# Performance work log

Hardware: AMD Instinct MI355X
Metric: run time of the kernel (lower is better)

## Reference

```python
import jax, jax.numpy as jnp
import numpy as np

B, S, D = 2, 2048, 1024
H = 16
HD = D // H  # 64
FORESIGHT = -1e9  # masked_fill value for non-causal positions


def setup_inputs() -> dict:
    key = jax.random.key(0)
    ks = jax.random.split(key, 8)
    s = 0.02
    return {
        "x": jax.random.normal(ks[0], (B, S, D), dtype=jnp.float32),
        "Wq": jax.random.normal(ks[1], (D, H * HD), dtype=jnp.float32) * s,
        "bq": jax.random.normal(ks[2], (H * HD,), dtype=jnp.float32) * s,
        "Wk": jax.random.normal(ks[3], (D, H * HD), dtype=jnp.float32) * s,
        "Wv": jax.random.normal(ks[4], (D, H * HD), dtype=jnp.float32) * s,
        "Wo": jax.random.normal(ks[5], (H * HD, D), dtype=jnp.float32) * s,
        "bo": jax.random.normal(ks[6], (D,), dtype=jnp.float32) * s,
    }


def reference(x, Wq, bq, Wk, Wv, Wo, bo):
    b, s, _ = x.shape
    # projections -> [B, H, S, HD]
    q = (x @ Wq + bq).reshape(b, s, H, HD).transpose(0, 2, 1, 3)
    k = (x @ Wk).reshape(b, s, H, HD).transpose(0, 2, 1, 3)
    v = (x @ Wv).reshape(b, s, H, HD).transpose(0, 2, 1, 3)
    # scores [B, H, S, S]
    scores = jnp.einsum("bhqd,bhkd->bhqk", q, k) / jnp.sqrt(jnp.float32(HD))
    # ALiBi bias: slope_h * j (key position), broadcast over queries
    slopes = 2.0 ** (-8.0 * jnp.arange(1, H + 1, dtype=jnp.float32) / H)
    positions = jnp.arange(s, dtype=jnp.float32)
    scores = scores - slopes[None, :, None, None] * positions[None, None, None, :]
    # causal mask: fill strictly-upper triangle with foresight
    causal = jnp.tril(jnp.ones((s, s), dtype=bool))
    scores = jnp.where(causal[None, None, :, :], scores, FORESIGHT)
    attn = jax.nn.softmax(scores, axis=-1)
    out = jnp.einsum("bhqk,bhkd->bhqd", attn, v)
    out = out.transpose(0, 2, 1, 3).reshape(b, s, H * HD)
    return out @ Wo + bo
```

## Files before the change

kernel.cpp:

```cpp
#include <hip/hip_runtime.h>
#include <stdint.h>

#define DDIM 1024
#define HH 16
#define HDIM 64
#define SS 2048
#define BB 2
#define MTOT 4096

typedef short bf16x8 __attribute__((ext_vector_type(8)));
typedef float f32x4 __attribute__((ext_vector_type(4)));
typedef unsigned short u16;

__device__ __forceinline__ u16 f2bf(float f) {
  unsigned u = __builtin_bit_cast(unsigned, f);
  u = u + 0x7FFFu + ((u >> 16) & 1u);
  return (u16)(u >> 16);
}

__device__ __forceinline__ void gload16(const void* g, void* l) {
  __builtin_amdgcn_global_load_lds(
      (const __attribute__((address_space(1))) unsigned int*)g,
      (__attribute__((address_space(3))) unsigned int*)l, 16, 0, 0);
}

__global__ void k_convert_x(const float* __restrict__ x, u16* __restrict__ xb) {
  int i = (blockIdx.x * 256 + threadIdx.x) * 4;
  float4 v = *(const float4*)(x + i);
  ushort4 o;
  o.x = f2bf(v.x); o.y = f2bf(v.y); o.z = f2bf(v.z); o.w = f2bf(v.w);
  *(ushort4*)(xb + i) = o;
}

__global__ void k_transpose_w(const float* __restrict__ w0, const float* __restrict__ w1,
                              const float* __restrict__ w2, const float* __restrict__ w3,
                              u16* __restrict__ wt) {
  __shared__ float t[64][65];
  int z = blockIdx.z;
  const float* src = (z == 0) ? w0 : (z == 1) ? w1 : (z == 2) ? w2 : w3;
  u16* dst = wt + (size_t)z * DDIM * DDIM;
  int k0 = blockIdx.x * 64, n0 = blockIdx.y * 64;
  int tid = threadIdx.x;
  int c4 = tid & 15, rr = tid >> 4;
  for (int rep = 0; rep < 4; rep++) {
    int r = rr + rep * 16;
    float4 v = *(const float4*)(src + (size_t)(k0 + r) * DDIM + n0 + c4 * 4);
    t[r][c4 * 4 + 0] = v.x; t[r][c4 * 4 + 1] = v.y;
    t[r][c4 * 4 + 2] = v.z; t[r][c4 * 4 + 3] = v.w;
  }
  __syncthreads();
  for (int rep = 0; rep < 4; rep++) {
    int n = rr + rep * 16;
    ushort4 o;
    o.x = f2bf(t[c4 * 4 + 0][n]); o.y = f2bf(t[c4 * 4 + 1][n]);
    o.z = f2bf(t[c4 * 4 + 2][n]); o.w = f2bf(t[c4 * 4 + 3][n]);
    *(ushort4*)(dst + (size_t)(n0 + n) * DDIM + k0 + c4 * 4) = o;
  }
}

template <int MODE>
__global__ __launch_bounds__(256, 2) void k_gemm(const u16* __restrict__ A,
                                                 const u16* __restrict__ BT,
                                                 const float* __restrict__ bias,
                                                 void* __restrict__ Cout) {
  __shared__ __align__(16) u16 lA[128 * 64];
  __shared__ __align__(16) u16 lB[128 * 64];
  const int tid = threadIdx.x;
  const int l = tid & 63, w = tid >> 6;
  const int wm = w >> 1, wn = w & 1;
  const int m0 = blockIdx.x * 128, n0 = blockIdx.y * 128;
  const int lr = l >> 4, lc = l & 15;

  const int srow = l >> 3;
  const int scol = ((l & 7) ^ srow) * 8;

  f32x4 acc[4][4];
  for (int mi = 0; mi < 4; mi++)
    for (int ni = 0; ni < 4; ni++)
      acc[mi][ni] = f32x4{0.f, 0.f, 0.f, 0.f};

  for (int kk = 0; kk < 16; kk++) {
    const int k0 = kk * 64;
    for (int i = 0; i < 4; i++) {
      int c = w * 4 + i;
      gload16(A + (size_t)(m0 + c * 8 + srow) * DDIM + k0 + scol, (char*)lA + c * 1024);
      gload16(BT + (size_t)(n0 + c * 8 + srow) * DDIM + k0 + scol, (char*)lB + c * 1024);
    }
    __syncthreads();
    for (int ks = 0; ks < 2; ks++) {
      bf16x8 af[4], bfr[4];
      for (int mi = 0; mi < 4; mi++) {
        int row = wm * 64 + mi * 16 + lc;
        int slot = (ks * 4 + lr) ^ (row & 7);
        af[mi] = *(const bf16x8*)((const char*)lA + row * 128 + slot * 16);
      }
      for (int ni = 0; ni < 4; ni++) {
        int row = wn * 64 + ni * 16 + lc;
        int slot = (ks * 4 + lr) ^ (row & 7);
        bfr[ni] = *(const bf16x8*)((const char*)lB + row * 128 + slot * 16);
      }
      for (int mi = 0; mi < 4; mi++)
        for (int ni = 0; ni < 4; ni++)
          acc[mi][ni] = __builtin_amdgcn_mfma_f32_16x16x32_bf16(af[mi], bfr[ni], acc[mi][ni], 0, 0, 0);
    }
    __syncthreads();
  }

  if (MODE == 0) {
    u16* C = (u16*)Cout;
    for (int mi = 0; mi < 4; mi++)
      for (int ni = 0; ni < 4; ni++) {
        int n = n0 + wn * 64 + ni * 16 + lc;
        float badd = bias ? bias[n] : 0.f;
        for (int r = 0; r < 4; r++) {
          int m = m0 + wm * 64 + mi * 16 + lr * 4 + r;
          C[(size_t)m * DDIM + n] = f2bf(acc[mi][ni][r] + badd);
        }
      }
  } else if (MODE == 1) {
    u16* C = (u16*)Cout;
    for (int mi = 0; mi < 4; mi++)
      for (int ni = 0; ni < 4; ni++) {
        int n = n0 + wn * 64 + ni * 16 + lc;
        int h = n >> 6, hd = n & 63;
        for (int r = 0; r < 4; r++) {
          int m = m0 + wm * 64 + mi * 16 + lr * 4 + r;
          int b = m >> 11, s = m & 2047;
          C[((size_t)((b * HH + h) * HDIM + hd)) * SS + s] = f2bf(acc[mi][ni][r]);
        }
      }
  } else {
    float* C = (float*)Cout;
    for (int mi = 0; mi < 4; mi++)
      for (int ni = 0; ni < 4; ni++) {
        int n = n0 + wn * 64 + ni * 16 + lc;
        float badd = bias[n];
        for (int r = 0; r < 4; r++) {
          int m = m0 + wm * 64 + mi * 16 + lr * 4 + r;
          C[(size_t)m * DDIM + n] = acc[mi][ni][r] + badd;
        }
      }
  }
}

__global__ __launch_bounds__(256, 3) void k_attn(const u16* __restrict__ Q,
                                                 const u16* __restrict__ Kg,
                                                 const u16* __restrict__ Vt,
                                                 u16* __restrict__ AO) {
  __shared__ __align__(16) u16 lK[128 * 64];
  __shared__ __align__(16) u16 lV[64 * 128];
  __shared__ __align__(16) u16 lP[4][16 * 128];

  const int tid = threadIdx.x;
  const int l = tid & 63, w = tid >> 6;
  const int lr = l >> 4, lc = l & 15;
  const int bh = blockIdx.x;
  const int b = bh >> 4, h = bh & 15;
  const int yq = blockIdx.y;
  const int fk = yq & 7, fj = yq >> 3;
  const int qt = (fj == 0) ? fk : (fj == 1) ? (15 - fk) : (fj == 2) ? (16 + fk) : (31 - fk);

  const float slope = exp2f(-0.5f * (float)(h + 1));
  const int q_glob = qt * 64 + w * 16 + lc;

  bf16x8 qf[2];
  for (int ks = 0; ks < 2; ks++)
    qf[ks] = *(const bf16x8*)(Q + (size_t)(b * SS + q_glob) * DDIM + h * HDIM + ks * 32 + lr * 8);

  f32x4 of[4];
  for (int mf = 0; mf < 4; mf++) of[mf] = f32x4{0.f, 0.f, 0.f, 0.f};
  float mrun = -INFINITY, lrun = 0.f;

  const int srowK = l >> 3;
  const int scolK = ((l & 7) ^ srowK) * 8;
  const int nkt = qt / 2 + 1;

  for (int kt = 0; kt < nkt; kt++) {
    for (int i = 0; i < 4; i++) {
      int c = w * 4 + i;
      int key = kt * 128 + c * 8 + srowK;
      gload16(Kg + (size_t)(b * SS + key) * DDIM + h * HDIM + scolK, (char*)lK + c * 1024);
      int hd = c * 4 + lr;
      int slot = (l & 15) ^ (hd & 7);
      gload16(Vt + ((size_t)bh * HDIM + hd) * SS + kt * 128 + slot * 8, (char*)lV + c * 1024);
    }
    __syncthreads();

    f32x4 sf[8];
    for (int kf = 0; kf < 8; kf++) sf[kf] = f32x4{0.f, 0.f, 0.f, 0.f};
    for (int ks = 0; ks < 2; ks++)
      for (int kf = 0; kf < 8; kf++) {
        int key = kf * 16 + lc;
        int slot = (ks * 4 + lr) ^ (key & 7);
        bf16x8 a = *(const bf16x8*)((const char*)lK + key * 128 + slot * 16);
        sf[kf] = __builtin_amdgcn_mfma_f32_16x16x32_bf16(a, qf[ks], sf[kf], 0, 0, 0);
      }

    float tmax = -INFINITY;
    for (int kf = 0; kf < 8; kf++)
      for (int r = 0; r < 4; r++) {
        int key = kt * 128 + kf * 16 + lr * 4 + r;
        float sv = sf[kf][r] * 0.125f - slope * (float)key;
        sv = (key > q_glob) ? -1e9f : sv;
        sf[kf][r] = sv;
        tmax = fmaxf(tmax, sv);
      }
    tmax = fmaxf(tmax, __shfl_xor(tmax, 16));
    tmax = fmaxf(tmax, __shfl_xor(tmax, 32));
    float mnew = fmaxf(mrun, tmax);
    float scale = __expf(mrun - mnew);
    lrun *= scale;
    for (int mf = 0; mf < 4; mf++)
      for (int r = 0; r < 4; r++) of[mf][r] *= scale;

    float psum = 0.f;
    for (int kf = 0; kf < 8; kf++)
      for (int r = 0; r < 4; r++) {
        float p = __expf(sf[kf][r] - mnew);
        psum += p;
        int key = kf * 16 + lr * 4 + r;
        int slot = (key >> 3) ^ (lc & 7);
        *(u16*)((char*)lP[w] + lc * 256 + slot * 16 + (key & 7) * 2) = f2bf(p);
      }
    psum += __shfl_xor(psum, 16);
    psum += __shfl_xor(psum, 32);
    lrun += psum;
    mrun = mnew;

    for (int ks = 0; ks < 4; ks++) {
      int slotp = (ks * 4 + lr) ^ (lc & 7);
      bf16x8 pb = *(const bf16x8*)((const char*)lP[w] + lc * 256 + slotp * 16);
      for (int mf = 0; mf < 4; mf++) {
        int hd = mf * 16 + lc;
        int slotv = (ks * 4 + lr) ^ (hd & 7);
        bf16x8 va = *(const bf16x8*)((const char*)lV + hd * 256 + slotv * 16);
        of[mf] = __builtin_amdgcn_mfma_f32_16x16x32_bf16(va, pb, of[mf], 0, 0, 0);
      }
    }
    __syncthreads();
  }

  float inv = 1.f / lrun;
  for (int mf = 0; mf < 4; mf++)
    for (int r = 0; r < 4; r++) {
      int hd = mf * 16 + lr * 4 + r;
      AO[(size_t)(b * SS + q_glob) * DDIM + h * HDIM + hd] = f2bf(of[mf][r] * inv);
    }
}

extern "C" void kernel_launch(void* const* d_in, const int* in_sizes, int n_in,
                              void* d_out, int out_size, void* d_ws, size_t ws_size,
                              hipStream_t stream) {
  const float* x  = (const float*)d_in[0];
  const float* Wq = (const float*)d_in[1];
  const float* bq = (const float*)d_in[2];
  const float* Wk = (const float*)d_in[3];
  const float* Wv = (const float*)d_in[4];
  const float* Wo = (const float*)d_in[5];
  const float* bo = (const float*)d_in[6];
  float* out = (float*)d_out;

  u16* ws = (u16*)d_ws;
  const size_t MEG = 1024 * 1024;
  u16* xb = ws;
  u16* WT = ws + 4 * MEG;
  u16* Qb = ws + 8 * MEG;
  u16* Kb = ws + 12 * MEG;
  u16* Vt = ws + 16 * MEG;
  u16* AO = ws + 20 * MEG;

  k_convert_x<<<dim3(4096), dim3(256), 0, stream>>>(x, xb);
  k_transpose_w<<<dim3(16, 16, 4), dim3(256), 0, stream>>>(Wq, Wk, Wv, Wo, WT);
  k_gemm<0><<<dim3(32, 8), dim3(256), 0, stream>>>(xb, WT + 0 * MEG, bq, (void*)Qb);
  k_gemm<0><<<dim3(32, 8), dim3(256), 0, stream>>>(xb, WT + 1 * MEG, (const float*)nullptr, (void*)Kb);
  k_gemm<1><<<dim3(32, 8), dim3(256), 0, stream>>>(xb, WT + 2 * MEG, (const float*)nullptr, (void*)Vt);
  k_attn<<<dim3(32, 32), dim3(256), 0, stream>>>(Qb, Kb, Vt, AO);
  k_gemm<2><<<dim3(32, 8), dim3(256), 0, stream>>>(AO, WT + 3 * MEG, bo, (void*)out);
}
```

Measured before the change: 151.2 us.

## Fuse QKV GEMMs, keep P in registers, skip masked tiles in attention

Merges the three QKV projection launches into one grid of 24 column tiles that writes Q, K and transposed V, with V stored as packed 32-bit pairs. The attention kernel no longer routes P through LDS: it packs the probabilities into bf16x4 registers and feeds them to 16x16x16 MFMAs. Only the last key tile is masked, and for even query tiles half of its key fragments are skipped. The rescale runs only when the running max grows, the output is written with vector stores, and the occupancy hint rises to 4. This cuts kernel launches, LDS traffic and wasted masked work, at the cost of more inline asm and register pressure.

Result: faster. 123.7 us (-18.2%).

```diff
diff --git a/kernel.cpp b/kernel.cpp
--- a/kernel.cpp
+++ b/kernel.cpp
@@ -5,17 +5,20 @@
 #define HH 16
 #define HDIM 64
 #define SS 2048
-#define BB 2
-#define MTOT 4096
 
 typedef short bf16x8 __attribute__((ext_vector_type(8)));
+typedef short bf16x4 __attribute__((ext_vector_type(4)));
 typedef float f32x4 __attribute__((ext_vector_type(4)));
 typedef unsigned short u16;
 
-__device__ __forceinline__ u16 f2bf(float f) {
+__device__ __forceinline__ unsigned f2bf(float f) {
   unsigned u = __builtin_bit_cast(unsigned, f);
   u = u + 0x7FFFu + ((u >> 16) & 1u);
-  return (u16)(u >> 16);
+  return u >> 16;
+}
+
+__device__ __forceinline__ void mfma16(f32x4& c, bf16x4 a, bf16x4 b) {
+  asm("v_mfma_f32_16x16x16_bf16 %0, %1, %2, %0" : "+v"(c) : "v"(a), "v"(b));
 }
 
 __device__ __forceinline__ void gload16(const void* g, void* l) {
@@ -28,7 +31,7 @@
   int i = (blockIdx.x * 256 + threadIdx.x) * 4;
   float4 v = *(const float4*)(x + i);
   ushort4 o;
-  o.x = f2bf(v.x); o.y = f2bf(v.y); o.z = f2bf(v.z); o.w = f2bf(v.w);
+  o.x = (u16)f2bf(v.x); o.y = (u16)f2bf(v.y); o.z = (u16)f2bf(v.z); o.w = (u16)f2bf(v.w);
   *(ushort4*)(xb + i) = o;
 }
 
@@ -52,8 +55,8 @@
   for (int rep = 0; rep < 4; rep++) {
     int n = rr + rep * 16;
     ushort4 o;
-    o.x = f2bf(t[c4 * 4 + 0][n]); o.y = f2bf(t[c4 * 4 + 1][n]);
-    o.z = f2bf(t[c4 * 4 + 2][n]); o.w = f2bf(t[c4 * 4 + 3][n]);
+    o.x = (u16)f2bf(t[c4 * 4 + 0][n]); o.y = (u16)f2bf(t[c4 * 4 + 1][n]);
+    o.z = (u16)f2bf(t[c4 * 4 + 2][n]); o.w = (u16)f2bf(t[c4 * 4 + 3][n]);
     *(ushort4*)(dst + (size_t)(n0 + n) * DDIM + k0 + c4 * 4) = o;
   }
 }
@@ -62,7 +65,9 @@
 __global__ __launch_bounds__(256, 2) void k_gemm(const u16* __restrict__ A,
                                                  const u16* __restrict__ BT,
                                                  const float* __restrict__ bias,
-                                                 void* __restrict__ Cout) {
+                                                 void* __restrict__ O0,
+                                                 void* __restrict__ O1,
+                                                 void* __restrict__ O2) {
   __shared__ __align__(16) u16 lA[128 * 64];
   __shared__ __align__(16) u16 lB[128 * 64];
   const int tid = threadIdx.x;
@@ -107,30 +112,45 @@
   }
 
   if (MODE == 0) {
-    u16* C = (u16*)Cout;
-    for (int mi = 0; mi < 4; mi++)
-      for (int ni = 0; ni < 4; ni++) {
-        int n = n0 + wn * 64 + ni * 16 + lc;
-        float badd = bias ? bias[n] : 0.f;
-        for (int r = 0; r < 4; r++) {
-          int m = m0 + wm * 64 + mi * 16 + lr * 4 + r;
-          C[(size_t)m * DDIM + n] = f2bf(acc[mi][ni][r] + badd);
+    const int which = blockIdx.y >> 3;
+    if (which == 0) {
+      u16* C = (u16*)O0;
+      for (int mi = 0; mi < 4; mi++)
+        for (int ni = 0; ni < 4; ni++) {
+          int nl = (n0 + wn * 64 + ni * 16 + lc) & 1023;
+          float badd = bias[nl];
+          for (int r = 0; r < 4; r++) {
+            int m = m0 + wm * 64 + mi * 16 + lr * 4 + r;
+            C[(size_t)m * DDIM + nl] = (u16)f2bf(acc[mi][ni][r] + badd);
+          }
         }
-      }
-  } else if (MODE == 1) {
-    u16* C = (u16*)Cout;
-    for (int mi = 0; mi < 4; mi++)
-      for (int ni = 0; ni < 4; ni++) {
-        int n = n0 + wn * 64 + ni * 16 + lc;
-        int h = n >> 6, hd = n & 63;
-        for (int r = 0; r < 4; r++) {
-          int m = m0 + wm * 64 + mi * 16 + lr * 4 + r;
+    } else if (which == 1) {
+      u16* C = (u16*)O1;
+      for (int mi = 0; mi < 4; mi++)
+        for (int ni = 0; ni < 4; ni++) {
+          int nl = (n0 + wn * 64 + ni * 16 + lc) & 1023;
+          for (int r = 0; r < 4; r++) {
+            int m = m0 + wm * 64 + mi * 16 + lr * 4 + r;
+            C[(size_t)m * DDIM + nl] = (u16)f2bf(acc[mi][ni][r]);
+          }
+        }
+    } else {
+      u16* C = (u16*)O2;
+      for (int mi = 0; mi < 4; mi++)
+        for (int ni = 0; ni < 4; ni++) {
+          int nl = (n0 + wn * 64 + ni * 16 + lc) & 1023;
+          int h = nl >> 6, hd = nl & 63;
+          int m = m0 + wm * 64 + mi * 16 + lr * 4;
           int b = m >> 11, s = m & 2047;
-          C[((size_t)((b * HH + h) * HDIM + hd)) * SS + s] = f2bf(acc[mi][ni][r]);
+          unsigned d0 = f2bf(acc[mi][ni][0]) | (f2bf(acc[mi][ni][1]) << 16);
+          unsigned d1 = f2bf(acc[mi][ni][2]) | (f2bf(acc[mi][ni][3]) << 16);
+          u16* p = C + ((size_t)((b * HH + h) * HDIM + hd)) * SS + s;
+          *(unsigned*)(p) = d0;
+          *(unsigned*)(p + 2) = d1;
         }
-      }
+    }
   } else {
-    float* C = (float*)Cout;
+    float* C = (float*)O0;
     for (int mi = 0; mi < 4; mi++)
       for (int ni = 0; ni < 4; ni++) {
         int n = n0 + wn * 64 + ni * 16 + lc;
@@ -143,13 +163,94 @@
   }
 }
 
-__global__ __launch_bounds__(256, 3) void k_attn(const u16* __restrict__ Q,
+__device__ __forceinline__ void attn_tile(int kt, bool masked, int kfhi,
+                                          const char* lKc, const char* lVc,
+                                          const bf16x8 qf[2], f32x4 of[4],
+                                          float& mrun, float& lrun,
+                                          float slope, int lr, int lc, int q_glob) {
+  f32x4 sf[8];
+#pragma unroll
+  for (int kf = 0; kf < 8; kf++) sf[kf] = f32x4{0.f, 0.f, 0.f, 0.f};
+#pragma unroll
+  for (int ks = 0; ks < 2; ks++)
+#pragma unroll
+    for (int kf = 0; kf < 8; kf++) {
+      if (kf >= kfhi) continue;
+      int key = kf * 16 + lc;
+      int slot = (ks * 4 + lr) ^ (lc & 7);
+      bf16x8 a = *(const bf16x8*)(lKc + key * 128 + slot * 16);
+      sf[kf] = __builtin_amdgcn_mfma_f32_16x16x32_bf16(a, qf[ks], sf[kf], 0, 0, 0);
+    }
+
+  float tmax = -INFINITY;
+#pragma unroll
+  for (int kf = 0; kf < 8; kf++) {
+    if (kf >= kfhi) continue;
+#pragma unroll
+    for (int r = 0; r < 4; r++) {
+      int key = kt * 128 + kf * 16 + lr * 4 + r;
+      float sv = sf[kf][r] * 0.125f - slope * (float)key;
+      if (masked && key > q_glob) sv = -1e9f;
+      sf[kf][r] = sv;
+      tmax = fmaxf(tmax, sv);
+    }
+  }
+  tmax = fmaxf(tmax, __shfl_xor(tmax, 16));
+  tmax = fmaxf(tmax, __shfl_xor(tmax, 32));
+
+  if (tmax > mrun) {
+    float corr = __expf(mrun - tmax);
+    lrun *= corr;
+#pragma unroll
+    for (int mf = 0; mf < 4; mf++) {
+      of[mf][0] *= corr; of[mf][1] *= corr; of[mf][2] *= corr; of[mf][3] *= corr;
+    }
+    mrun = tmax;
+  }
+
+  f32x4 ps = f32x4{0.f, 0.f, 0.f, 0.f};
+  bf16x4 pb[8];
+#pragma unroll
+  for (int kf = 0; kf < 8; kf++) {
+    if (kf >= kfhi) continue;
+    unsigned a0 = f2bf(__expf(sf[kf][0] - mrun));
+    unsigned a1 = f2bf(__expf(sf[kf][1] - mrun));
+    unsigned a2 = f2bf(__expf(sf[kf][2] - mrun));
+    unsigned a3 = f2bf(__expf(sf[kf][3] - mrun));
+    uint2 uu;
+    uu.x = a0 | (a1 << 16);
+    uu.y = a2 | (a3 << 16);
+    pb[kf] = __builtin_bit_cast(bf16x4, uu);
+    ps[0] += __builtin_bit_cast(float, a0 << 16);
+    ps[1] += __builtin_bit_cast(float, a1 << 16);
+    ps[2] += __builtin_bit_cast(float, a2 << 16);
+    ps[3] += __builtin_bit_cast(float, a3 << 16);
+  }
+  float psum = (ps[0] + ps[1]) + (ps[2] + ps[3]);
+  psum += __shfl_xor(psum, 16);
+  psum += __shfl_xor(psum, 32);
+  lrun += psum;
+
+#pragma unroll
+  for (int kf = 0; kf < 8; kf++) {
+    if (kf >= kfhi) continue;
+    int g2 = (kf << 1) + (lr >> 1);
+#pragma unroll
+    for (int mf = 0; mf < 4; mf++) {
+      int hd = mf * 16 + lc;
+      int byte = hd * 256 + ((g2 ^ (hd & 7)) << 4) + ((lr & 1) << 3);
+      bf16x4 va = *(const bf16x4*)(lVc + byte);
+      mfma16(of[mf], va, pb[kf]);
+    }
+  }
+}
+
+__global__ __launch_bounds__(256, 4) void k_attn(const u16* __restrict__ Q,
                                                  const u16* __restrict__ Kg,
                                                  const u16* __restrict__ Vt,
                                                  u16* __restrict__ AO) {
   __shared__ __align__(16) u16 lK[128 * 64];
   __shared__ __align__(16) u16 lV[64 * 128];
-  __shared__ __align__(16) u16 lP[4][16 * 128];
 
   const int tid = threadIdx.x;
   const int l = tid & 63, w = tid >> 6;
@@ -164,10 +265,12 @@
   const int q_glob = qt * 64 + w * 16 + lc;
 
   bf16x8 qf[2];
+#pragma unroll
   for (int ks = 0; ks < 2; ks++)
     qf[ks] = *(const bf16x8*)(Q + (size_t)(b * SS + q_glob) * DDIM + h * HDIM + ks * 32 + lr * 8);
 
   f32x4 of[4];
+#pragma unroll
   for (int mf = 0; mf < 4; mf++) of[mf] = f32x4{0.f, 0.f, 0.f, 0.f};
   float mrun = -INFINITY, lrun = 0.f;
 
@@ -175,77 +278,43 @@
   const int scolK = ((l & 7) ^ srowK) * 8;
   const int nkt = qt / 2 + 1;
 
-  for (int kt = 0; kt < nkt; kt++) {
+  auto stage = [&](int kt) {
+#pragma unroll
     for (int i = 0; i < 4; i++) {
       int c = w * 4 + i;
-      int key = kt * 128 + c * 8 + srowK;
-      gload16(Kg + (size_t)(b * SS + key) * DDIM + h * HDIM + scolK, (char*)lK + c * 1024);
+      gload16(Kg + (size_t)(b * SS + kt * 128 + c * 8 + srowK) * DDIM + h * HDIM + scolK,
+              (char*)lK + c * 1024);
       int hd = c * 4 + lr;
-      int slot = (l & 15) ^ (hd & 7);
-      gload16(Vt + ((size_t)bh * HDIM + hd) * SS + kt * 128 + slot * 8, (char*)lV + c * 1024);
-    }
+      gload16(Vt + ((size_t)bh * HDIM + hd) * SS + kt * 128 + (((l & 15) ^ (hd & 7)) << 3),
+              (char*)lV + c * 1024);
+    }
+  };
+
+  for (int kt = 0; kt < nkt - 1; kt++) {
+    stage(kt);
     __syncthreads();
-
-    f32x4 sf[8];
-    for (int kf = 0; kf < 8; kf++) sf[kf] = f32x4{0.f, 0.f, 0.f, 0.f};
-    for (int ks = 0; ks < 2; ks++)
-      for (int kf = 0; kf < 8; kf++) {
-        int key = kf * 16 + lc;
-        int slot = (ks * 4 + lr) ^ (key & 7);
-        bf16x8 a = *(const bf16x8*)((const char*)lK + key * 128 + slot * 16);
-        sf[kf] = __builtin_amdgcn_mfma_f32_16x16x32_bf16(a, qf[ks], sf[kf], 0, 0, 0);
-      }
-
-    float tmax = -INFINITY;
-    for (int kf = 0; kf < 8; kf++)
-      for (int r = 0; r < 4; r++) {
-        int key = kt * 128 + kf * 16 + lr * 4 + r;
-        float sv = sf[kf][r] * 0.125f - slope * (float)key;
-        sv = (key > q_glob) ? -1e9f : sv;
-        sf[kf][r] = sv;
-        tmax = fmaxf(tmax, sv);
-      }
-    tmax = fmaxf(tmax, __shfl_xor(tmax, 16));
-    tmax = fmaxf(tmax, __shfl_xor(tmax, 32));
-    float mnew = fmaxf(mrun, tmax);
-    float scale = __expf(mrun - mnew);
-    lrun *= scale;
-    for (int mf = 0; mf < 4; mf++)
-      for (int r = 0; r < 4; r++) of[mf][r] *= scale;
-
-    float psum = 0.f;
-    for (int kf = 0; kf < 8; kf++)
-      for (int r = 0; r < 4; r++) {
-        float p = __expf(sf[kf][r] - mnew);
-        psum += p;
-        int key = kf * 16 + lr * 4 + r;
-        int slot = (key >> 3) ^ (lc & 7);
-        *(u16*)((char*)lP[w] + lc * 256 + slot * 16 + (key & 7) * 2) = f2bf(p);
-      }
-    psum += __shfl_xor(psum, 16);
-    psum += __shfl_xor(psum, 32);
-    lrun += psum;
-    mrun = mnew;
-
-    for (int ks = 0; ks < 4; ks++) {
-      int slotp = (ks * 4 + lr) ^ (lc & 7);
-      bf16x8 pb = *(const bf16x8*)((const char*)lP[w] + lc * 256 + slotp * 16);
-      for (int mf = 0; mf < 4; mf++) {
-        int hd = mf * 16 + lc;
-        int slotv = (ks * 4 + lr) ^ (hd & 7);
-        bf16x8 va = *(const bf16x8*)((const char*)lV + hd * 256 + slotv * 16);
-        of[mf] = __builtin_amdgcn_mfma_f32_16x16x32_bf16(va, pb, of[mf], 0, 0, 0);
-      }
-    }
+    attn_tile(kt, false, 8, (const char*)lK, (const char*)lV, qf, of, mrun, lrun,
+              slope, lr, lc, q_glob);
     __syncthreads();
   }
+  stage(nkt - 1);
+  __syncthreads();
+  if (qt & 1)
+    attn_tile(nkt - 1, true, 8, (const char*)lK, (const char*)lV, qf, of, mrun, lrun,
+              slope, lr, lc, q_glob);
+  else
+    attn_tile(nkt - 1, true, 4, (const char*)lK, (const char*)lV, qf, of, mrun, lrun,
+              slope, lr, lc, q_glob);
 
   float inv = 1.f / lrun;
-  for (int mf = 0; mf < 4; mf++)
-    for (int r = 0; r < 4; r++) {
-      int hd = mf * 16 + lr * 4 + r;
-      AO[(size_t)(b * SS + q_glob) * DDIM + h * HDIM + hd] = f2bf(of[mf][r] * inv);
-    }
+  u16* obase = AO + (size_t)(b * SS + q_glob) * DDIM + h * HDIM;
+#pragma unroll
+  for (int mf = 0; mf < 4; mf++) {
+    uint2 uu;
+    uu.x = f2bf(of[mf][0] * inv) | (f2bf(of[mf][1] * inv) << 16);
+    uu.y = f2bf(of[mf][2] * inv) | (f2bf(of[mf][3] * inv) << 16);
+    *(uint2*)(obase + mf * 16 + lr * 4) = uu;
+  }
 }
 
 extern "C" void kernel_launch(void* const* d_in, const int* in_sizes, int n_in,
@@ -271,9 +340,7 @@
 
   k_convert_x<<<dim3(4096), dim3(256), 0, stream>>>(x, xb);
   k_transpose_w<<<dim3(16, 16, 4), dim3(256), 0, stream>>>(Wq, Wk, Wv, Wo, WT);
-  k_gemm<0><<<dim3(32, 8), dim3(256), 0, stream>>>(xb, WT + 0 * MEG, bq, (void*)Qb);
-  k_gemm<0><<<dim3(32, 8), dim3(256), 0, stream>>>(xb, WT + 1 * MEG, (const float*)nullptr, (void*)Kb);
-  k_gemm<1><<<dim3(32, 8), dim3(256), 0, stream>>>(xb, WT + 2 * MEG, (const float*)nullptr, (void*)Vt);
+  k_gemm<0><<<dim3(32, 24), dim3(256), 0, stream>>>(xb, WT, bq, (void*)Qb, (void*)Kb, (void*)Vt);
   k_attn<<<dim3(32, 32), dim3(256), 0, stream>>>(Qb, Kb, Vt, AO);
-  k_gemm<2><<<dim3(32, 8), dim3(256), 0, stream>>>(AO, WT + 3 * MEG, bo, (void*)out);
-}
+  k_gemm<1><<<dim3(32, 8), dim3(256), 0, stream>>>(AO, WT + 3 * MEG, bo, (void*)out, nullptr, nullptr);
+}
```
